# Optimization experiments

Hardware: AMD Instinct MI355X
Metric: run time of the kernel (lower is better)

Reference implementation:

```python
import jax, jax.numpy as jnp
import numpy as np

N_NODES = 1024
E_EDGES = 4096
P_DEG = 5


def setup_inputs() -> dict:
    rng = np.random.default_rng(0)
    N, E = N_NODES, E_EDGES
    # graph incidence matrix: column j has +1 at node n_j, -1 at node m_j
    n_idx = rng.integers(0, N, size=E)
    m_idx = (n_idx + 1 + rng.integers(0, N - 1, size=E)) % N  # guarantees n != m
    B = np.zeros((N, E), dtype=np.float32)
    B[n_idx, np.arange(E)] = 1.0
    B[m_idx, np.arange(E)] = -1.0
    edges = np.stack([n_idx, m_idx], axis=1).astype(np.int32)

    key = jax.random.key(0)
    kq, ky, ks = jax.random.split(key, 3)
    q = jax.random.normal(kq, (N,), dtype=jnp.float32)
    y = jax.random.normal(ky, (N,), dtype=jnp.float32)
    s0 = jax.random.uniform(ks, (E,), dtype=jnp.float32) + 0.1  # positive edge weights

    F = 0.99 * jnp.eye(E, dtype=jnp.float32)          # state transition (E x E)
    C_u = 1e-2 * jnp.eye(E, dtype=jnp.float32)        # process noise
    C_w = 1e-1 * jnp.eye(N, dtype=jnp.float32)        # measurement noise
    Sigma0 = jnp.eye(E, dtype=jnp.float32)            # initial state covariance
    a = jnp.array([0.0, 1.0, 0.5, 0.25, 0.1], dtype=jnp.float32)  # poly coeffs, P=5

    return {"q": q, "y": y, "F": F, "B": jnp.asarray(B), "edges": jnp.asarray(edges),
            "C_u": C_u, "C_w": C_w, "s0": s0, "Sigma0": Sigma0, "a": a}


def _ekf_step(q, y, F, B, edges, C_u, C_w, s0, Sigma0, a):
    N = q.shape[0]
    P = a.shape[0]
    dt = q.dtype

    # ---- predict ----
    s = F @ s0
    Sigma = F @ Sigma0 @ F.T + C_u

    # ---- update ----
    # L = B diag(s) B^T  (weighted graph Laplacian)
    L = (B * s[None, :]) @ B.T  # (N, N)

    # c[p] = L^p q  (forward recursion)
    def c_step(cp, _):
        cn = L @ cp
        return cn, cn
    _, cs = jax.lax.scan(c_step, q, None, length=P - 1)
    c = jnp.concatenate([q[None, :], cs], axis=0)  # (P, N)

    # D[P-1] = 0;  D[p] = L @ D[p+1] + a[p+1] * I  (backward recursion)
    I_N = jnp.eye(N, dtype=dt)
    def d_step(Dn, ap1):
        Dp = L @ Dn + ap1 * I_N
        return Dp, Dp
    _, Ds = jax.lax.scan(d_step, jnp.zeros((N, N), dtype=dt), a[1:][::-1])
    # Ds[k] = D[P-2-k] -> reorder to D[0..P-1], append D[P-1]=0
    D = jnp.concatenate([Ds[::-1], jnp.zeros((1, N, N), dtype=dt)], axis=0)  # (P, N, N)

    # edge-indexed gather, vectorized over all edges
    n_i = edges[:, 0]
    m_i = edges[:, 1]
    dc = c[:, n_i] - c[:, m_i]          # (P, E)
    dD = D[:, :, n_i] - D[:, :, m_i]    # (P, N, E)
    H = jnp.einsum('pe,pne->ne', dc, dD)  # Jacobian (N, E)

    # Kalman gain (solve instead of explicit inverse; S symmetric)
    S = H @ Sigma @ H.T + C_w                 # (N, N)
    PHt = Sigma @ H.T                          # (E, N)
    K = jnp.linalg.solve(S, PHt.T).T           # (E, N)

    # innovation uses compute_poly(L, q, a) = sum_p a_p L^p q = sum_p a_p c[p]
    f_pred = jnp.einsum('p,pn->n', a, c)
    s_new = s + K @ (y - f_pred)

    # Joseph-form covariance update (computed as in base class; not returned)
    I_E = jnp.eye(s.shape[0], dtype=dt)
    IKH = I_E - K @ H
    Sigma_new = IKH @ Sigma @ IKH.T + K @ C_w @ K.T

    s_out = jnp.maximum(s_new, 0.0)
    return s_out, Sigma_new


def reference(q, y, F, B, edges, C_u, C_w, s0, Sigma0, a):
    s_out, _ = _ekf_step(q, y, F, B, edges, C_u, C_w, s0, Sigma0, a)
    return s_out
```

## Files before the change

### kernel.cpp

```cpp
#include <hip/hip_runtime.h>

#define NN 1024
#define EE 4096
#define CAP 64
#define BD 64
#define NB 16
#define KSPLIT 4
#define NTILE 136
#define NSLOT 200
#define GFACT 122

__device__ __forceinline__ double waveReduceD(double v){
  for (int o = 32; o; o >>= 1) v += __shfl_down(v, o, 64);
  return v;
}
__device__ __forceinline__ double agld(const double* p){
  return __hip_atomic_load(p, __ATOMIC_RELAXED, __HIP_MEMORY_SCOPE_AGENT);
}
__device__ __forceinline__ void agst(double* p, double v){
  __hip_atomic_store(p, v, __ATOMIC_RELAXED, __HIP_MEMORY_SCOPE_AGENT);
}

__global__ __launch_bounds__(1024) void k_prep(const float* __restrict__ F, const float* __restrict__ Sg0,
                                               const float* __restrict__ Cu, const float* __restrict__ s0,
                                               const int* __restrict__ edges, const float* __restrict__ q,
                                               const float* __restrict__ y, const float* __restrict__ a,
                                               float* __restrict__ sv, float* __restrict__ sg,
                                               float* __restrict__ L, int* __restrict__ cnt,
                                               int* __restrict__ nb, float* __restrict__ wg,
                                               float* __restrict__ bt, double* __restrict__ rz){
  __shared__ int scnt[NN];
  __shared__ float cbs[5][NN];
  int tid = threadIdx.x;
  scnt[tid] = 0;
  __syncthreads();
  for (int e = tid; e < EE; e += 1024){
    float f = F[(size_t)e*EE + e];
    float se = f * s0[e];
    sv[e] = se;
    sg[e] = f*f*Sg0[(size_t)e*EE + e] + Cu[(size_t)e*EE + e];
    int n = edges[2*e], m = edges[2*e+1];
    atomicAdd(&L[(size_t)n*NN + n],  se);
    atomicAdd(&L[(size_t)m*NN + m],  se);
    atomicAdd(&L[(size_t)n*NN + m], -se);
    atomicAdd(&L[(size_t)m*NN + n], -se);
    int p1 = atomicAdd(&scnt[n], 1);
    if (p1 < CAP){ nb[n*CAP+p1] = m; wg[n*CAP+p1] = se; }
    int p2 = atomicAdd(&scnt[m], 1);
    if (p2 < CAP){ nb[m*CAP+p2] = n; wg[m*CAP+p2] = se; }
  }
  __syncthreads();
  cnt[tid] = scnt[tid];
  cbs[0][tid] = q[tid];
  __syncthreads();
  for (int p = 1; p < 5; ++p){
    float acc = L[(size_t)tid*NN + tid] * cbs[p-1][tid];
    int c = min(scnt[tid], CAP);
    for (int t = 0; t < c; ++t) acc -= wg[tid*CAP+t] * cbs[p-1][nb[tid*CAP+t]];
    cbs[p][tid] = acc;
    __syncthreads();
  }
  float a1 = a[1], a2 = a[2], a3 = a[3], a4 = a[4];
  for (int e = tid; e < EE; e += 1024){
    int n = edges[2*e], m = edges[2*e+1];
    float dc0 = cbs[0][n]-cbs[0][m], dc1 = cbs[1][n]-cbs[1][m];
    float dc2 = cbs[2][n]-cbs[2][m], dc3 = cbs[3][n]-cbs[3][m];
    bt[e]      = dc0*a1 + dc1*a2 + dc2*a3 + dc3*a4;
    bt[EE+e]   = dc0*a2 + dc1*a3 + dc2*a4;
    bt[2*EE+e] = dc0*a3 + dc1*a4;
    bt[3*EE+e] = dc0*a4;
  }
  double acc = (double)y[tid];
  float a0 = a[0];
  acc -= (double)a0*cbs[0][tid]; acc -= (double)a1*cbs[1][tid];
  acc -= (double)a2*cbs[2][tid]; acc -= (double)a3*cbs[3][tid];
  acc -= (double)a4*cbs[4][tid];
  rz[tid] = acc;
}

__global__ __launch_bounds__(256) void k_srow(const float* __restrict__ L, const int* __restrict__ cnt,
                                              const int* __restrict__ nb, const float* __restrict__ wg,
                                              const float* __restrict__ X, float* __restrict__ Y){
  int i = blockIdx.x;
  __shared__ int   snb[CAP];
  __shared__ float swt[CAP];
  __shared__ float sdiag;
  int c = min(cnt[i], CAP);
  if ((int)threadIdx.x < c){ snb[threadIdx.x] = nb[i*CAP+threadIdx.x]; swt[threadIdx.x] = wg[i*CAP+threadIdx.x]; }
  if (threadIdx.x == 0) sdiag = L[(size_t)i*NN + i];
  __syncthreads();
  for (int j = threadIdx.x; j < NN; j += 256){
    float acc = sdiag * X[(size_t)i*NN + j];
    for (int t = 0; t < c; ++t) acc -= swt[t] * X[(size_t)snb[t]*NN + j];
    Y[(size_t)i*NN + j] = acc;
  }
}

__global__ __launch_bounds__(256) void k_hbuild(const int* __restrict__ edges, const float* __restrict__ bt,
                                                const float* __restrict__ L, const float* __restrict__ L2,
                                                const float* __restrict__ L3, float* __restrict__ Ht){
  int e = blockIdx.x;
  int n = edges[2*e], m = edges[2*e+1];
  float b0 = bt[e], b1 = bt[EE+e], b2 = bt[2*EE+e], b3 = bt[3*EE+e];
  const float* Ln  = L  + (size_t)n*NN; const float* Lm  = L  + (size_t)m*NN;
  const float* L2n = L2 + (size_t)n*NN; const float* L2m = L2 + (size_t)m*NN;
  const float* L3n = L3 + (size_t)n*NN; const float* L3m = L3 + (size_t)m*NN;
  float* He = Ht + (size_t)e*NN;
  for (int j = threadIdx.x; j < NN; j += 256){
    float v = b1*(Ln[j]-Lm[j]) + b2*(L2n[j]-L2m[j]) + b3*(L3n[j]-L3m[j]);
    if (j == n) v += b0;
    if (j == m) v -= b0;
    He[j] = v;
  }
}

__device__ __forceinline__ void tri_decode(int p, int& ti, int& tj){
  ti = (int)((sqrtf(8.f*p + 1.f) - 1.f)*0.5f);
  while ((ti+1)*(ti+2)/2 <= p) ti++;
  while (ti*(ti+1)/2 > p) ti--;
  tj = p - ti*(ti+1)/2;
}

__global__ __launch_bounds__(256,2) void k_sgemm2(const float* __restrict__ Ht, const float* __restrict__ sg,
                                                  double* __restrict__ Spart){
  int p = blockIdx.x, z = blockIdx.y;
  int ti, tj; tri_decode(p, ti, tj);
  int i0 = ti*64, j0 = tj*64;
  __shared__ double As[32][66];
  __shared__ double Bs[32][66];
  int tid = threadIdx.x;
  int tx = tid & 15, ty = tid >> 4;
  double acc[4][4] = {};
  int kbase = z*(EE/KSPLIT);
  for (int k0 = kbase; k0 < kbase + EE/KSPLIT; k0 += 32){
#pragma unroll
    for (int l = 0; l < 2; ++l){
      int s = tid + 256*l;
      int kk = s >> 4, g = s & 15;
      const float* row = Ht + (size_t)(k0+kk)*NN;
      float4 va = *(const float4*)(row + i0 + g*4);
      float4 vb = *(const float4*)(row + j0 + g*4);
      double sgd = (double)sg[k0+kk];
      As[kk][g*4+0] = (double)va.x; As[kk][g*4+1] = (double)va.y;
      As[kk][g*4+2] = (double)va.z; As[kk][g*4+3] = (double)va.w;
      Bs[kk][g*4+0] = (double)vb.x*sgd; Bs[kk][g*4+1] = (double)vb.y*sgd;
      Bs[kk][g*4+2] = (double)vb.z*sgd; Bs[kk][g*4+3] = (double)vb.w*sgd;
    }
    __syncthreads();
#pragma unroll
    for (int kk = 0; kk < 32; ++kk){
      double av[4], bv[4];
#pragma unroll
      for (int q = 0; q < 4; ++q){ av[q] = As[kk][tx*4+q]; bv[q] = Bs[kk][ty*4+q]; }
#pragma unroll
      for (int r = 0; r < 4; ++r)
#pragma unroll
        for (int c = 0; c < 4; ++c)
          acc[r][c] += av[r]*bv[c];
    }
    __syncthreads();
  }
  double* out = Spart + ((size_t)z*NTILE + p)*4096;
#pragma unroll
  for (int r = 0; r < 4; ++r)
#pragma unroll
    for (int c = 0; c < 4; ++c)
      out[(tx*4+r)*64 + ty*4+c] = acc[r][c];
}

__global__ __launch_bounds__(256,1) void k_fact(const double* __restrict__ Spart, const float* __restrict__ Cw,
                                                double* __restrict__ Sd, double* __restrict__ rz,
                                                double* __restrict__ grd, double* __restrict__ dvals,
                                                int* __restrict__ fl){
  __shared__ double T[BD][BD+1];
  __shared__ double R[BD][BD+1];
  __shared__ double dsh[BD];
  __shared__ double zsh[BD];
  int bid = blockIdx.x, tid = threadIdx.x;
  int tx = tid & 15, ty = tid >> 4;
  int lane = tid & 63, wv = tid >> 6;

  auto poll_one = [&](int slot){
    int it = 0;
    while (__hip_atomic_load(&fl[slot*16], __ATOMIC_RELAXED, __HIP_MEMORY_SCOPE_AGENT) == 0 && it < 30000000){
      __builtin_amdgcn_s_sleep(2); ++it;
    }
  };
  auto wait2 = [&](int s1, int s2){
    if (tid == 0){ poll_one(s1); if (s2 >= 0) poll_one(s2); }
    __syncthreads();
  };
  auto set_slot = [&](int slot){
    __syncthreads();
    if (tid == 0)
      __hip_atomic_store(&fl[slot*16], 1, __ATOMIC_RELAXED, __HIP_MEMORY_SCOPE_AGENT);
  };
  auto pslotf = [](int X, int tt){ return (X == tt+1) ? (16+tt) : (32 + (X-1)*(X-2)/2 + tt); };

  auto load_acc = [&](int pidx, int gi, int gj, double (&acc)[4][4]){
    const double* sp = Spart + (size_t)pidx*4096;
#pragma unroll
    for (int q2 = 0; q2 < 4; ++q2)
#pragma unroll
      for (int p2 = 0; p2 < 4; ++p2){
        int idx = (tx*4+q2)*64 + ty*4+p2;
        double v = (double)Cw[(size_t)(gi+tx*4+q2)*NN + gj+ty*4+p2];
        v += sp[idx];
        v += sp[(size_t)NTILE*4096 + idx];
        v += sp[(size_t)2*NTILE*4096 + idx];
        v += sp[(size_t)3*NTILE*4096 + idx];
        acc[q2][p2] = v;
      }
  };
  auto upd = [&](double (&acc)[4][4]){
    for (int k = 0; k < BD; ++k){
      double av[4], bv[4];
#pragma unroll
      for (int q2 = 0; q2 < 4; ++q2){ av[q2] = T[tx*4+q2][k]; bv[q2] = R[ty*4+q2][k]; }
#pragma unroll
      for (int r = 0; r < 4; ++r)
#pragma unroll
        for (int c = 0; c < 4; ++c)
          acc[r][c] -= av[r]*bv[c];
    }
  };
  auto ldT = [&](int row64, int col64){
    for (int idx = tid; idx < 4096; idx += 256){
      int r = idx >> 6, c = idx & 63;
      T[r][c] = agld(&Sd[(size_t)(row64+r)*NN + col64 + c]);
    }
  };

  auto factor64 = [&](int off){
    if (tid < 64){
      double r_[64];
#pragma unroll
      for (int k = 0; k < 64; ++k) r_[k] = T[tid][k];
      double myd = 0.0;
#pragma unroll
      for (int j = 0; j < 64; ++j){
        double d = __shfl(r_[j], j, 64);
        double l = r_[j]/d;
        double lm = (tid > j) ? l : 0.0;
        if (tid == j) myd = d;
#pragma unroll
        for (int k = j+1; k < 64; ++k){
          double p = __shfl(r_[k], j, 64);
          r_[k] -= lm*p;
        }
        if (tid > j) r_[j] = l;
      }
      double myinv = 1.0/myd;
#pragma unroll
      for (int k = 0; k < 64; ++k) if (k > tid) r_[k] *= myinv;
#pragma unroll
      for (int k = 0; k < 64; ++k) T[tid][k] = r_[k];
      dsh[tid] = myinv;
      agst(&grd[off+tid], myinv);
      agst(&dvals[off+tid], myd);
    }
    __syncthreads();
  };
  auto trsm64 = [&](){
    if (tid < 64){
      double x_[64];
#pragma unroll
      for (int k = 0; k < 64; ++k) x_[k] = R[tid][k];
#pragma unroll
      for (int j = 1; j < 64; ++j){
        double a2 = x_[j];
#pragma unroll
        for (int k = 0; k < j; ++k) a2 -= x_[k]*T[j][k];
        x_[j] = a2;
      }
#pragma unroll
      for (int k = 0; k < 64; ++k) R[tid][k] = x_[k]*dsh[k];
    }
    __syncthreads();
  };

  if (bid < NB){
    int t = bid, t64 = t*64, u64 = t64+64;
    double accD[4][4], accP[4][4];
    load_acc(t*(t+1)/2 + t, t64, t64, accD);
    if (t < 15) load_acc((t+1)*(t+2)/2 + t, u64, t64, accP);
    for (int tt = 0; tt < t; ++tt){
      int tt64 = tt*64;
      wait2(pslotf(t,tt), -1);
      if (tid < 64) dsh[tid] = agld(&dvals[tt64+tid]);
      ldT(t64, tt64);
      __syncthreads();
      for (int idx = tid; idx < 4096; idx += 256){
        int r = idx >> 6, c = idx & 63;
        R[r][c] = T[r][c]*dsh[c];
      }
      __syncthreads();
      upd(accD);
      __syncthreads();
      if (t < 15){
        wait2(pslotf(t+1,tt), -1);
        ldT(u64, tt64);
        __syncthreads();
        upd(accP);
        __syncthreads();
      }
    }
#pragma unroll
    for (int q2 = 0; q2 < 4; ++q2)
#pragma unroll
      for (int p2 = 0; p2 < 4; ++p2) T[tx*4+q2][ty*4+p2] = accD[q2][p2];
    __syncthreads();
    factor64(t64);
    for (int idx = tid; idx < 4096; idx += 256){
      int r = idx >> 6, c = idx & 63;
      agst(&Sd[(size_t)(t64+r)*NN + t64 + c], T[r][c]);
    }
    set_slot(t);
    if (t < 15){
#pragma unroll
      for (int q2 = 0; q2 < 4; ++q2)
#pragma unroll
        for (int p2 = 0; p2 < 4; ++p2) R[tx*4+q2][ty*4+p2] = accP[q2][p2];
      __syncthreads();
      trsm64();
      for (int idx = tid; idx < 4096; idx += 256){
        int r = idx >> 6, c = idx & 63;
        agst(&Sd[(size_t)(u64+r)*NN + t64 + c], R[r][c]);
      }
      set_slot(16+t);
    }
  } else if (bid < NB + 105){
    int q = bid - NB;
    int I = 2;
    for (int ii = 3; ii <= 15; ++ii) if ((ii-1)*(ii-2)/2 <= q) I = ii;
    int J = q - (I-1)*(I-2)/2;
    int i64 = I*64, j64 = J*64;
    double acc[4][4];
    load_acc(I*(I+1)/2 + J, i64, j64, acc);
    for (int tt = 0; tt < J; ++tt){
      int tt64 = tt*64;
      wait2(pslotf(I,tt), pslotf(J,tt));
      if (tid < 64) dsh[tid] = agld(&dvals[tt64+tid]);
      __syncthreads();
      for (int idx = tid; idx < 4096; idx += 256){
        int r = idx >> 6, c = idx & 63;
        T[r][c] = agld(&Sd[(size_t)(i64+r)*NN + tt64 + c]);
        R[r][c] = agld(&Sd[(size_t)(j64+r)*NN + tt64 + c]) * dsh[c];
      }
      __syncthreads();
      upd(acc);
      __syncthreads();
    }
    wait2(J, -1);
    ldT(j64, j64);
    if (tid < 64) dsh[tid] = agld(&grd[j64+tid]);
    __syncthreads();
#pragma unroll
    for (int q2 = 0; q2 < 4; ++q2)
#pragma unroll
      for (int p2 = 0; p2 < 4; ++p2) R[tx*4+q2][ty*4+p2] = acc[q2][p2];
    __syncthreads();
    trsm64();
    for (int idx = tid; idx < 4096; idx += 256){
      int r = idx >> 6, c = idx & 63;
      agst(&Sd[(size_t)(i64+r)*NN + j64 + c], R[r][c]);
    }
    set_slot(32 + (I-1)*(I-2)/2 + J);
  } else {
    for (int t = 0; t < NB; ++t){
      int t64 = t*64;
      {
        int I = t+2+tid;
        if (I <= 15) poll_one(32 + (I-1)*(I-2)/2 + t);
        if (tid == 0){ poll_one(t); if (t < 15) poll_one(16+t); }
      }
      __syncthreads();
      for (int idx = tid; idx < BD*BD; idx += 256){
        int r = idx >> 6, c = idx & 63;
        T[r][c] = agld(&Sd[(size_t)(t64+r)*NN + t64 + c]);
      }
      __syncthreads();
      if (wv == 0){
        double x = rz[t64 + lane];
        for (int j = 0; j < BD-1; ++j){
          double xj = __shfl(x, j, 64);
          if (lane > j) x -= T[j][lane]*xj;
        }
        zsh[lane] = x;
        rz[t64 + lane] = x;
      }
      __syncthreads();
      for (int g0 = t64 + BD + wv*4; g0 < NN; g0 += 16){
        double v0 = agld(&Sd[(size_t)(g0+0)*NN + t64 + lane])*zsh[lane];
        double v1 = agld(&Sd[(size_t)(g0+1)*NN + t64 + lane])*zsh[lane];
        double v2 = agld(&Sd[(size_t)(g0+2)*NN + t64 + lane])*zsh[lane];
        double v3 = agld(&Sd[(size_t)(g0+3)*NN + t64 + lane])*zsh[lane];
        v0 = waveReduceD(v0); v1 = waveReduceD(v1);
        v2 = waveReduceD(v2); v3 = waveReduceD(v3);
        if (lane == 0){
          rz[g0+0] -= v0; rz[g0+1] -= v1; rz[g0+2] -= v2; rz[g0+3] -= v3;
        }
      }
      __syncthreads();
    }
    for (int i = tid; i < NN; i += 256) rz[i] *= agld(&grd[i]);
    __syncthreads();
    for (int t = NB-1; t >= 0; --t){
      int t64 = t*64;
      for (int idx = tid; idx < BD*BD; idx += 256){
        int r = idx >> 6, c = idx & 63;
        T[r][c] = agld(&Sd[(size_t)(t64+r)*NN + t64 + c]);
      }
      __syncthreads();
      if (wv == 0){
        double x = rz[t64 + lane];
        for (int j = BD-1; j >= 1; --j){
          double xj = __shfl(x, j, 64);
          if (lane < j) x -= T[j][lane]*xj;
        }
        zsh[lane] = x;
        rz[t64 + lane] = x;
      }
      __syncthreads();
      for (int J = wv; J < t; J += 4){
        int j64 = J*64;
        double a2 = 0.0;
#pragma unroll 8
        for (int r = 0; r < 64; ++r)
          a2 += agld(&Sd[(size_t)(t64+r)*NN + j64 + lane]) * zsh[r];
        rz[j64+lane] -= a2;
      }
      __syncthreads();
    }
  }
}

__global__ __launch_bounds__(256) void k_snew(const float* __restrict__ Ht, const float* __restrict__ sv,
                                              const float* __restrict__ sg, const double* __restrict__ z,
                                              float* __restrict__ out){
  int e = blockIdx.x*4 + (threadIdx.x >> 6);
  int lane = threadIdx.x & 63;
  const float* He = Ht + (size_t)e*NN;
  double acc = 0.0;
  for (int j = lane; j < NN; j += 64) acc += (double)He[j]*z[j];
  acc = waveReduceD(acc);
  if (lane == 0){
    double val = (double)sv[e] + (double)sg[e]*acc;
    out[e] = fmaxf((float)val, 0.0f);
  }
}

extern "C" void kernel_launch(void* const* d_in, const int* in_sizes, int n_in,
                              void* d_out, int out_size, void* d_ws, size_t ws_size,
                              hipStream_t stream){
  const float* q   = (const float*)d_in[0];
  const float* y   = (const float*)d_in[1];
  const float* F   = (const float*)d_in[2];
  const int*   edges = (const int*)d_in[4];
  const float* Cu  = (const float*)d_in[5];
  const float* Cw  = (const float*)d_in[6];
  const float* s0  = (const float*)d_in[7];
  const float* Sg0 = (const float*)d_in[8];
  const float* a   = (const float*)d_in[9];
  float* out = (float*)d_out;

  double* Sd    = (double*)d_ws;
  double* Spart = Sd + (size_t)NN*NN;
  double* rz    = Spart + (size_t)KSPLIT*NTILE*4096;
  double* grd   = rz + NN;
  double* dvals = grd + NN;
  float* w = (float*)(dvals + NN);
  float* L  = w; w += (size_t)NN*NN;
  float* L2 = w; w += (size_t)NN*NN;
  float* L3 = w; w += (size_t)NN*NN;
  float* Ht = w; w += (size_t)EE*NN;
  float* sv = w; w += EE;
  float* sg = w; w += EE;
  float* bt = w; w += 4*EE;
  float* wg = w; w += (size_t)NN*CAP;
  int* cnt  = (int*)w; w += NN;
  int* nb   = (int*)w; w += (size_t)NN*CAP;
  int* fl   = (int*)w; w += NSLOT*16;

  hipMemsetAsync(L, 0, (size_t)NN*NN*sizeof(float), stream);
  hipMemsetAsync(fl, 0, NSLOT*16*sizeof(int), stream);

  k_prep<<<1, 1024, 0, stream>>>(F, Sg0, Cu, s0, edges, q, y, a,
                                 sv, sg, L, cnt, nb, wg, bt, rz);

  k_srow<<<NN, 256, 0, stream>>>(L, cnt, nb, wg, L,  L2);
  k_srow<<<NN, 256, 0, stream>>>(L, cnt, nb, wg, L2, L3);
  k_hbuild<<<EE, 256, 0, stream>>>(edges, bt, L, L2, L3, Ht);

  dim3 gg(NTILE, KSPLIT);
  k_sgemm2<<<gg, 256, 0, stream>>>(Ht, sg, Spart);

  k_fact<<<GFACT, 256, 0, stream>>>(Spart, Cw, Sd, rz, grd, dvals, fl);

  k_snew<<<EE/4, 256, 0, stream>>>(Ht, sv, sg, rz, out);
}
```

Baseline: 1.639 ms.

## Widen factorization blocks to 1024 threads and split triangular solve into own kernel

The blocked LDL^T factorization kernel now runs 1024 threads per block, so each thread holds a 2x2 accumulator instead of 4x4 and the tile loads and stores are spread over more threads. The forward/backward triangular solve that used to run in a dedicated polling block overlapped with the factorization is moved to a separate single-block kernel launched afterward. That kernel uses 1024 threads and plain loads instead of atomic loads. This gives more parallelism per tile and removes the solve's flag polling. In exchange it loses the overlap of the solve with the factorization and adds one kernel launch. The factor64 and trsm64 helpers, which are only partly visible, still assume thread indices below 64 and must work with the larger blocks.

```diff
diff --git a/kernel.cpp b/kernel.cpp
--- a/kernel.cpp
+++ b/kernel.cpp
@@ -8,7 +8,7 @@
 #define KSPLIT 4
 #define NTILE 136
 #define NSLOT 200
-#define GFACT 122
+#define GFACT 121
 
 __device__ __forceinline__ double waveReduceD(double v){
   for (int o = 32; o; o >>= 1) v += __shfl_down(v, o, 64);
@@ -168,17 +168,15 @@
       out[(tx*4+r)*64 + ty*4+c] = acc[r][c];
 }
 
-__global__ __launch_bounds__(256,1) void k_fact(const double* __restrict__ Spart, const float* __restrict__ Cw,
-                                                double* __restrict__ Sd, double* __restrict__ rz,
-                                                double* __restrict__ grd, double* __restrict__ dvals,
-                                                int* __restrict__ fl){
+__global__ __launch_bounds__(1024,1) void k_fact(const double* __restrict__ Spart, const float* __restrict__ Cw,
+                                                 double* __restrict__ Sd,
+                                                 double* __restrict__ grd, double* __restrict__ dvals,
+                                                 int* __restrict__ fl){
   __shared__ double T[BD][BD+1];
   __shared__ double R[BD][BD+1];
   __shared__ double dsh[BD];
-  __shared__ double zsh[BD];
   int bid = blockIdx.x, tid = threadIdx.x;
-  int tx = tid & 15, ty = tid >> 4;
-  int lane = tid & 63, wv = tid >> 6;
+  int tx = tid & 31, ty = tid >> 5;
 
   auto poll_one = [&](int slot){
     int it = 0;
@@ -197,14 +195,14 @@
   };
   auto pslotf = [](int X, int tt){ return (X == tt+1) ? (16+tt) : (32 + (X-1)*(X-2)/2 + tt); };
 
-  auto load_acc = [&](int pidx, int gi, int gj, double (&acc)[4][4]){
+  auto load_acc = [&](int pidx, int gi, int gj, double (&acc)[2][2]){
     const double* sp = Spart + (size_t)pidx*4096;
 #pragma unroll
-    for (int q2 = 0; q2 < 4; ++q2)
-#pragma unroll
-      for (int p2 = 0; p2 < 4; ++p2){
-        int idx = (tx*4+q2)*64 + ty*4+p2;
-        double v = (double)Cw[(size_t)(gi+tx*4+q2)*NN + gj+ty*4+p2];
+    for (int q2 = 0; q2 < 2; ++q2)
+#pragma unroll
+      for (int p2 = 0; p2 < 2; ++p2){
+        int idx = (tx*2+q2)*64 + ty*2+p2;
+        double v = (double)Cw[(size_t)(gi+tx*2+q2)*NN + gj+ty*2+p2];
         v += sp[idx];
         v += sp[(size_t)NTILE*4096 + idx];
         v += sp[(size_t)2*NTILE*4096 + idx];
@@ -212,20 +210,20 @@
         acc[q2][p2] = v;
       }
   };
-  auto upd = [&](double (&acc)[4][4]){
+  auto upd = [&](double (&acc)[2][2]){
     for (int k = 0; k < BD; ++k){
-      double av[4], bv[4];
-#pragma unroll
-      for (int q2 = 0; q2 < 4; ++q2){ av[q2] = T[tx*4+q2][k]; bv[q2] = R[ty*4+q2][k]; }
-#pragma unroll
-      for (int r = 0; r < 4; ++r)
-#pragma unroll
-        for (int c = 0; c < 4; ++c)
+      double av[2], bv[2];
+#pragma unroll
+      for (int q2 = 0; q2 < 2; ++q2){ av[q2] = T[tx*2+q2][k]; bv[q2] = R[ty*2+q2][k]; }
+#pragma unroll
+      for (int r = 0; r < 2; ++r)
+#pragma unroll
+        for (int c = 0; c < 2; ++c)
           acc[r][c] -= av[r]*bv[c];
     }
   };
   auto ldT = [&](int row64, int col64){
-    for (int idx = tid; idx < 4096; idx += 256){
+    for (int idx = tid; idx < 4096; idx += 1024){
       int r = idx >> 6, c = idx & 63;
       T[r][c] = agld(&Sd[(size_t)(row64+r)*NN + col64 + c]);
     }
@@ -281,7 +279,7 @@
 
   if (bid < NB){
     int t = bid, t64 = t*64, u64 = t64+64;
-    double accD[4][4], accP[4][4];
+    double accD[2][2], accP[2][2];
     load_acc(t*(t+1)/2 + t, t64, t64, accD);
     if (t < 15) load_acc((t+1)*(t+2)/2 + t, u64, t64, accP);
     for (int tt = 0; tt < t; ++tt){
@@ -290,7 +288,7 @@
       if (tid < 64) dsh[tid] = agld(&dvals[tt64+tid]);
       ldT(t64, tt64);
       __syncthreads();
-      for (int idx = tid; idx < 4096; idx += 256){
+      for (int idx = tid; idx < 4096; idx += 1024){
         int r = idx >> 6, c = idx & 63;
         R[r][c] = T[r][c]*dsh[c];
       }
@@ -306,43 +304,43 @@
       }
     }
 #pragma unroll
-    for (int q2 = 0; q2 < 4; ++q2)
-#pragma unroll
-      for (int p2 = 0; p2 < 4; ++p2) T[tx*4+q2][ty*4+p2] = accD[q2][p2];
+    for (int q2 = 0; q2 < 2; ++q2)
+#pragma unroll
+      for (int p2 = 0; p2 < 2; ++p2) T[tx*2+q2][ty*2+p2] = accD[q2][p2];
     __syncthreads();
     factor64(t64);
-    for (int idx = tid; idx < 4096; idx += 256){
+    for (int idx = tid; idx < 4096; idx += 1024){
       int r = idx >> 6, c = idx & 63;
       agst(&Sd[(size_t)(t64+r)*NN + t64 + c], T[r][c]);
     }
     set_slot(t);
     if (t < 15){
 #pragma unroll
-      for (int q2 = 0; q2 < 4; ++q2)
-#pragma unroll
-        for (int p2 = 0; p2 < 4; ++p2) R[tx*4+q2][ty*4+p2] = accP[q2][p2];
+      for (int q2 = 0; q2 < 2; ++q2)
+#pragma unroll
+        for (int p2 = 0; p2 < 2; ++p2) R[tx*2+q2][ty*2+p2] = accP[q2][p2];
       __syncthreads();
       trsm64();
-      for (int idx = tid; idx < 4096; idx += 256){
+      for (int idx = tid; idx < 4096; idx += 1024){
         int r = idx >> 6, c = idx & 63;
         agst(&Sd[(size_t)(u64+r)*NN + t64 + c], R[r][c]);
       }
       set_slot(16+t);
     }
-  } else if (bid < NB + 105){
+  } else {
     int q = bid - NB;
     int I = 2;
     for (int ii = 3; ii <= 15; ++ii) if ((ii-1)*(ii-2)/2 <= q) I = ii;
     int J = q - (I-1)*(I-2)/2;
     int i64 = I*64, j64 = J*64;
-    double acc[4][4];
+    double acc[2][2];
     load_acc(I*(I+1)/2 + J, i64, j64, acc);
     for (int tt = 0; tt < J; ++tt){
       int tt64 = tt*64;
       wait2(pslotf(I,tt), pslotf(J,tt));
       if (tid < 64) dsh[tid] = agld(&dvals[tt64+tid]);
       __syncthreads();
-      for (int idx = tid; idx < 4096; idx += 256){
+      for (int idx = tid; idx < 4096; idx += 1024){
         int r = idx >> 6, c = idx & 63;
         T[r][c] = agld(&Sd[(size_t)(i64+r)*NN + tt64 + c]);
         R[r][c] = agld(&Sd[(size_t)(j64+r)*NN + tt64 + c]) * dsh[c];
@@ -356,82 +354,82 @@
     if (tid < 64) dsh[tid] = agld(&grd[j64+tid]);
     __syncthreads();
 #pragma unroll
-    for (int q2 = 0; q2 < 4; ++q2)
-#pragma unroll
-      for (int p2 = 0; p2 < 4; ++p2) R[tx*4+q2][ty*4+p2] = acc[q2][p2];
+    for (int q2 = 0; q2 < 2; ++q2)
+#pragma unroll
+      for (int p2 = 0; p2 < 2; ++p2) R[tx*2+q2][ty*2+p2] = acc[q2][p2];
     __syncthreads();
     trsm64();
-    for (int idx = tid; idx < 4096; idx += 256){
+    for (int idx = tid; idx < 4096; idx += 1024){
       int r = idx >> 6, c = idx & 63;
       agst(&Sd[(size_t)(i64+r)*NN + j64 + c], R[r][c]);
     }
     set_slot(32 + (I-1)*(I-2)/2 + J);
-  } else {
-    for (int t = 0; t < NB; ++t){
-      int t64 = t*64;
-      {
-        int I = t+2+tid;
-        if (I <= 15) poll_one(32 + (I-1)*(I-2)/2 + t);
-        if (tid == 0){ poll_one(t); if (t < 15) poll_one(16+t); }
-      }
-      __syncthreads();
-      for (int idx = tid; idx < BD*BD; idx += 256){
-        int r = idx >> 6, c = idx & 63;
-        T[r][c] = agld(&Sd[(size_t)(t64+r)*NN + t64 + c]);
-      }
-      __syncthreads();
-      if (wv == 0){
-        double x = rz[t64 + lane];
-        for (int j = 0; j < BD-1; ++j){
-          double xj = __shfl(x, j, 64);
-          if (lane > j) x -= T[j][lane]*xj;
-        }
-        zsh[lane] = x;
-        rz[t64 + lane] = x;
-      }
-      __syncthreads();
-      for (int g0 = t64 + BD + wv*4; g0 < NN; g0 += 16){
-        double v0 = agld(&Sd[(size_t)(g0+0)*NN + t64 + lane])*zsh[lane];
-        double v1 = agld(&Sd[(size_t)(g0+1)*NN + t64 + lane])*zsh[lane];
-        double v2 = agld(&Sd[(size_t)(g0+2)*NN + t64 + lane])*zsh[lane];
-        double v3 = agld(&Sd[(size_t)(g0+3)*NN + t64 + lane])*zsh[lane];
-        v0 = waveReduceD(v0); v1 = waveReduceD(v1);
-        v2 = waveReduceD(v2); v3 = waveReduceD(v3);
-        if (lane == 0){
-          rz[g0+0] -= v0; rz[g0+1] -= v1; rz[g0+2] -= v2; rz[g0+3] -= v3;
-        }
-      }
-      __syncthreads();
-    }
-    for (int i = tid; i < NN; i += 256) rz[i] *= agld(&grd[i]);
-    __syncthreads();
-    for (int t = NB-1; t >= 0; --t){
-      int t64 = t*64;
-      for (int idx = tid; idx < BD*BD; idx += 256){
-        int r = idx >> 6, c = idx & 63;
-        T[r][c] = agld(&Sd[(size_t)(t64+r)*NN + t64 + c]);
-      }
-      __syncthreads();
-      if (wv == 0){
-        double x = rz[t64 + lane];
-        for (int j = BD-1; j >= 1; --j){
-          double xj = __shfl(x, j, 64);
-          if (lane < j) x -= T[j][lane]*xj;
-        }
-        zsh[lane] = x;
-        rz[t64 + lane] = x;
-      }
-      __syncthreads();
-      for (int J = wv; J < t; J += 4){
-        int j64 = J*64;
-        double a2 = 0.0;
+  }
+}
+
+__global__ __launch_bounds__(1024) void k_solve(const double* __restrict__ Sd, double* __restrict__ rz,
+                                                const double* __restrict__ grd){
+  __shared__ double T[BD][BD+1];
+  __shared__ double zsh[BD];
+  int tid = threadIdx.x, lane = tid & 63, wv = tid >> 6;
+  for (int t = 0; t < NB; ++t){
+    int t64 = t*64;
+    for (int idx = tid; idx < BD*BD; idx += 1024){
+      int r = idx >> 6, c = idx & 63;
+      T[r][c] = Sd[(size_t)(t64+r)*NN + t64 + c];
+    }
+    __syncthreads();
+    if (wv == 0){
+      double x = rz[t64 + lane];
+      for (int j = 0; j < BD-1; ++j){
+        double xj = __shfl(x, j, 64);
+        if (lane > j) x -= T[j][lane]*xj;
+      }
+      zsh[lane] = x;
+      rz[t64 + lane] = x;
+    }
+    __syncthreads();
+    for (int g0 = t64 + BD + wv*4; g0 < NN; g0 += 64){
+      double v0 = Sd[(size_t)(g0+0)*NN + t64 + lane]*zsh[lane];
+      double v1 = Sd[(size_t)(g0+1)*NN + t64 + lane]*zsh[lane];
+      double v2 = Sd[(size_t)(g0+2)*NN + t64 + lane]*zsh[lane];
+      double v3 = Sd[(size_t)(g0+3)*NN + t64 + lane]*zsh[lane];
+      v0 = waveReduceD(v0); v1 = waveReduceD(v1);
+      v2 = waveReduceD(v2); v3 = waveReduceD(v3);
+      if (lane == 0){
+        rz[g0+0] -= v0; rz[g0+1] -= v1; rz[g0+2] -= v2; rz[g0+3] -= v3;
+      }
+    }
+    __syncthreads();
+  }
+  rz[tid] *= grd[tid];
+  __syncthreads();
+  for (int t = NB-1; t >= 0; --t){
+    int t64 = t*64;
+    for (int idx = tid; idx < BD*BD; idx += 1024){
+      int r = idx >> 6, c = idx & 63;
+      T[r][c] = Sd[(size_t)(t64+r)*NN + t64 + c];
+    }
+    __syncthreads();
+    if (wv == 0){
+      double x = rz[t64 + lane];
+      for (int j = BD-1; j >= 1; --j){
+        double xj = __shfl(x, j, 64);
+        if (lane < j) x -= T[j][lane]*xj;
+      }
+      zsh[lane] = x;
+      rz[t64 + lane] = x;
+    }
+    __syncthreads();
+    for (int J = wv; J < t; J += 16){
+      int j64 = J*64;
+      double a2 = 0.0;
 #pragma unroll 8
-        for (int r = 0; r < 64; ++r)
-          a2 += agld(&Sd[(size_t)(t64+r)*NN + j64 + lane]) * zsh[r];
-        rz[j64+lane] -= a2;
-      }
-      __syncthreads();
-    }
+      for (int r = 0; r < 64; ++r)
+        a2 += Sd[(size_t)(t64+r)*NN + j64 + lane] * zsh[r];
+      rz[j64+lane] -= a2;
+    }
+    __syncthreads();
   }
 }
 
@@ -495,7 +493,8 @@
   dim3 gg(NTILE, KSPLIT);
   k_sgemm2<<<gg, 256, 0, stream>>>(Ht, sg, Spart);
 
-  k_fact<<<GFACT, 256, 0, stream>>>(Spart, Cw, Sd, rz, grd, dvals, fl);
+  k_fact<<<GFACT, 1024, 0, stream>>>(Spart, Cw, Sd, grd, dvals, fl);
+  k_solve<<<1, 1024, 0, stream>>>(Sd, rz, grd);
 
   k_snew<<<EE/4, 256, 0, stream>>>(Ht, sv, sg, rz, out);
 }
```

Measured after the change: 4.481 ms. 2.73x slower.

## Parallelize block LDL factor and trsm across block, split triangular solve into own kernel

Applied to the files above, without the earlier changes.

Replaces the single-wave register-resident 64x64 LDL factorization and triangular solve with versions that use all 256 threads through shared memory, in the column-chunked trsm form. Diagonal blocks now publish their factor before accumulating the sub-diagonal panel, which shortens the dependency chain for the other blocks. The forward and backward solve moves out of the persistent fused kernel into a separate 1024-thread launch, removing polling and atomic loads from that path. The cost is an extra kernel launch and more barriers inside the factor loop.

```diff
diff --git a/kernel.cpp b/kernel.cpp
--- a/kernel.cpp
+++ b/kernel.cpp
@@ -8,7 +8,7 @@
 #define KSPLIT 4
 #define NTILE 136
 #define NSLOT 200
-#define GFACT 122
+#define GFACT 121
 
 __device__ __forceinline__ double waveReduceD(double v){
   for (int o = 32; o; o >>= 1) v += __shfl_down(v, o, 64);
@@ -169,16 +169,14 @@
 }
 
 __global__ __launch_bounds__(256,1) void k_fact(const double* __restrict__ Spart, const float* __restrict__ Cw,
-                                                double* __restrict__ Sd, double* __restrict__ rz,
+                                                double* __restrict__ Sd,
                                                 double* __restrict__ grd, double* __restrict__ dvals,
                                                 int* __restrict__ fl){
   __shared__ double T[BD][BD+1];
   __shared__ double R[BD][BD+1];
   __shared__ double dsh[BD];
-  __shared__ double zsh[BD];
   int bid = blockIdx.x, tid = threadIdx.x;
   int tx = tid & 15, ty = tid >> 4;
-  int lane = tid & 63, wv = tid >> 6;
 
   auto poll_one = [&](int slot){
     int it = 0;
@@ -231,52 +229,48 @@
     }
   };
 
-  auto factor64 = [&](int off){
-    if (tid < 64){
-      double r_[64];
-#pragma unroll
-      for (int k = 0; k < 64; ++k) r_[k] = T[tid][k];
-      double myd = 0.0;
-#pragma unroll
-      for (int j = 0; j < 64; ++j){
-        double d = __shfl(r_[j], j, 64);
-        double l = r_[j]/d;
-        double lm = (tid > j) ? l : 0.0;
-        if (tid == j) myd = d;
-#pragma unroll
-        for (int k = j+1; k < 64; ++k){
-          double p = __shfl(r_[k], j, 64);
-          r_[k] -= lm*p;
+  auto factor_wb = [&](int off0){
+    __syncthreads();
+    for (int j = 0; j < BD; ++j){
+      double dj = T[j][j];
+      int fi = tid & 63, cg = tid >> 6;
+      if (fi > j){
+        double l = T[j][fi]/dj;
+        for (int c = j+1+cg; c < BD; c += 4) T[fi][c] -= l*T[j][c];
+      }
+      __syncthreads();
+    }
+    if (tid < BD) dsh[tid] = 1.0 / T[tid][tid];
+    __syncthreads();
+    for (int idx = tid; idx < BD*BD; idx += 256){
+      int r = idx >> 6, c = idx & 63;
+      double v = (r == c) ? T[r][r] : (r > c ? T[r][c]*dsh[c] : T[r][c]*dsh[r]);
+      agst(&Sd[(size_t)(off0+r)*NN + off0 + c], v);
+    }
+    if (tid < BD){ agst(&grd[off0+tid], dsh[tid]); agst(&dvals[off0+tid], 1.0/dsh[tid]); }
+  };
+  auto trsm_chunk = [&](){
+    for (int c0 = 0; c0 < BD; c0 += 16){
+      if (tid < BD){
+        for (int jj = 0; jj < 16; ++jj){
+          int j = c0 + jj;
+          double a2 = R[tid][j];
+          for (int k = 0; k < jj; ++k) a2 -= R[tid][c0+k]*T[j][c0+k];
+          R[tid][j] = a2;
         }
-        if (tid > j) r_[j] = l;
-      }
-      double myinv = 1.0/myd;
-#pragma unroll
-      for (int k = 0; k < 64; ++k) if (k > tid) r_[k] *= myinv;
-#pragma unroll
-      for (int k = 0; k < 64; ++k) T[tid][k] = r_[k];
-      dsh[tid] = myinv;
-      agst(&grd[off+tid], myinv);
-      agst(&dvals[off+tid], myd);
-    }
-    __syncthreads();
-  };
-  auto trsm64 = [&](){
-    if (tid < 64){
-      double x_[64];
-#pragma unroll
-      for (int k = 0; k < 64; ++k) x_[k] = R[tid][k];
-#pragma unroll
-      for (int j = 1; j < 64; ++j){
-        double a2 = x_[j];
-#pragma unroll
-        for (int k = 0; k < j; ++k) a2 -= x_[k]*T[j][k];
-        x_[j] = a2;
-      }
-#pragma unroll
-      for (int k = 0; k < 64; ++k) R[tid][k] = x_[k]*dsh[k];
-    }
-    __syncthreads();
+      }
+      __syncthreads();
+      if (c0 + 16 < BD){
+        int r2 = tid & 63, jg = tid >> 6;
+        for (int j = c0+16+jg; j < BD; j += 4){
+          double a2 = R[r2][j];
+#pragma unroll
+          for (int k = 0; k < 16; ++k) a2 -= R[r2][c0+k]*T[j][c0+k];
+          R[r2][j] = a2;
+        }
+        __syncthreads();
+      }
+    }
   };
 
   if (bid < NB){
@@ -297,39 +291,44 @@
       __syncthreads();
       upd(accD);
       __syncthreads();
-      if (t < 15){
+    }
+#pragma unroll
+    for (int q2 = 0; q2 < 4; ++q2)
+#pragma unroll
+      for (int p2 = 0; p2 < 4; ++p2) T[tx*4+q2][ty*4+p2] = accD[q2][p2];
+    factor_wb(t64);
+    set_slot(t);
+    if (t < 15){
+      for (int tt = 0; tt < t; ++tt){
+        int tt64 = tt*64;
         wait2(pslotf(t+1,tt), -1);
-        ldT(u64, tt64);
+        if (tid < 64) dsh[tid] = agld(&dvals[tt64+tid]);
+        __syncthreads();
+        for (int idx = tid; idx < 4096; idx += 256){
+          int r = idx >> 6, c = idx & 63;
+          T[r][c] = agld(&Sd[(size_t)(u64+r)*NN + tt64 + c]);
+          R[r][c] = agld(&Sd[(size_t)(t64+r)*NN + tt64 + c]) * dsh[c];
+        }
         __syncthreads();
         upd(accP);
         __syncthreads();
       }
-    }
-#pragma unroll
-    for (int q2 = 0; q2 < 4; ++q2)
-#pragma unroll
-      for (int p2 = 0; p2 < 4; ++p2) T[tx*4+q2][ty*4+p2] = accD[q2][p2];
-    __syncthreads();
-    factor64(t64);
-    for (int idx = tid; idx < 4096; idx += 256){
-      int r = idx >> 6, c = idx & 63;
-      agst(&Sd[(size_t)(t64+r)*NN + t64 + c], T[r][c]);
-    }
-    set_slot(t);
-    if (t < 15){
+      ldT(t64, t64);
+      if (tid < 64) dsh[tid] = agld(&grd[t64+tid]);
+      __syncthreads();
 #pragma unroll
       for (int q2 = 0; q2 < 4; ++q2)
 #pragma unroll
         for (int p2 = 0; p2 < 4; ++p2) R[tx*4+q2][ty*4+p2] = accP[q2][p2];
       __syncthreads();
-      trsm64();
+      trsm_chunk();
       for (int idx = tid; idx < 4096; idx += 256){
         int r = idx >> 6, c = idx & 63;
-        agst(&Sd[(size_t)(u64+r)*NN + t64 + c], R[r][c]);
+        agst(&Sd[(size_t)(u64+r)*NN + t64 + c], R[r][c]*dsh[c]);
       }
       set_slot(16+t);
     }
-  } else if (bid < NB + 105){
+  } else {
     int q = bid - NB;
     int I = 2;
     for (int ii = 3; ii <= 15; ++ii) if ((ii-1)*(ii-2)/2 <= q) I = ii;
@@ -360,78 +359,78 @@
 #pragma unroll
       for (int p2 = 0; p2 < 4; ++p2) R[tx*4+q2][ty*4+p2] = acc[q2][p2];
     __syncthreads();
-    trsm64();
+    trsm_chunk();
     for (int idx = tid; idx < 4096; idx += 256){
       int r = idx >> 6, c = idx & 63;
-      agst(&Sd[(size_t)(i64+r)*NN + j64 + c], R[r][c]);
+      agst(&Sd[(size_t)(i64+r)*NN + j64 + c], R[r][c]*dsh[c]);
     }
     set_slot(32 + (I-1)*(I-2)/2 + J);
-  } else {
-    for (int t = 0; t < NB; ++t){
-      int t64 = t*64;
-      {
-        int I = t+2+tid;
-        if (I <= 15) poll_one(32 + (I-1)*(I-2)/2 + t);
-        if (tid == 0){ poll_one(t); if (t < 15) poll_one(16+t); }
-      }
-      __syncthreads();
-      for (int idx = tid; idx < BD*BD; idx += 256){
-        int r = idx >> 6, c = idx & 63;
-        T[r][c] = agld(&Sd[(size_t)(t64+r)*NN + t64 + c]);
-      }
-      __syncthreads();
-      if (wv == 0){
-        double x = rz[t64 + lane];
-        for (int j = 0; j < BD-1; ++j){
-          double xj = __shfl(x, j, 64);
-          if (lane > j) x -= T[j][lane]*xj;
-        }
-        zsh[lane] = x;
-        rz[t64 + lane] = x;
-      }
-      __syncthreads();
-      for (int g0 = t64 + BD + wv*4; g0 < NN; g0 += 16){
-        double v0 = agld(&Sd[(size_t)(g0+0)*NN + t64 + lane])*zsh[lane];
-        double v1 = agld(&Sd[(size_t)(g0+1)*NN + t64 + lane])*zsh[lane];
-        double v2 = agld(&Sd[(size_t)(g0+2)*NN + t64 + lane])*zsh[lane];
-        double v3 = agld(&Sd[(size_t)(g0+3)*NN + t64 + lane])*zsh[lane];
-        v0 = waveReduceD(v0); v1 = waveReduceD(v1);
-        v2 = waveReduceD(v2); v3 = waveReduceD(v3);
-        if (lane == 0){
-          rz[g0+0] -= v0; rz[g0+1] -= v1; rz[g0+2] -= v2; rz[g0+3] -= v3;
-        }
-      }
-      __syncthreads();
-    }
-    for (int i = tid; i < NN; i += 256) rz[i] *= agld(&grd[i]);
-    __syncthreads();
-    for (int t = NB-1; t >= 0; --t){
-      int t64 = t*64;
-      for (int idx = tid; idx < BD*BD; idx += 256){
-        int r = idx >> 6, c = idx & 63;
-        T[r][c] = agld(&Sd[(size_t)(t64+r)*NN + t64 + c]);
-      }
-      __syncthreads();
-      if (wv == 0){
-        double x = rz[t64 + lane];
-        for (int j = BD-1; j >= 1; --j){
-          double xj = __shfl(x, j, 64);
-          if (lane < j) x -= T[j][lane]*xj;
-        }
-        zsh[lane] = x;
-        rz[t64 + lane] = x;
-      }
-      __syncthreads();
-      for (int J = wv; J < t; J += 4){
-        int j64 = J*64;
-        double a2 = 0.0;
+  }
+}
+
+__global__ __launch_bounds__(1024) void k_solve(const double* __restrict__ Sd, double* __restrict__ rz,
+                                                const double* __restrict__ grd){
+  __shared__ double T[BD][BD+1];
+  __shared__ double zsh[BD];
+  int tid = threadIdx.x, lane = tid & 63, wv = tid >> 6;
+  for (int t = 0; t < NB; ++t){
+    int t64 = t*64;
+    for (int idx = tid; idx < BD*BD; idx += 1024){
+      int r = idx >> 6, c = idx & 63;
+      T[r][c] = Sd[(size_t)(t64+r)*NN + t64 + c];
+    }
+    __syncthreads();
+    if (wv == 0){
+      double x = rz[t64 + lane];
+      for (int j = 0; j < BD-1; ++j){
+        double xj = __shfl(x, j, 64);
+        if (lane > j) x -= T[j][lane]*xj;
+      }
+      zsh[lane] = x;
+      rz[t64 + lane] = x;
+    }
+    __syncthreads();
+    for (int g0 = t64 + BD + wv*4; g0 < NN; g0 += 64){
+      double v0 = Sd[(size_t)(g0+0)*NN + t64 + lane]*zsh[lane];
+      double v1 = Sd[(size_t)(g0+1)*NN + t64 + lane]*zsh[lane];
+      double v2 = Sd[(size_t)(g0+2)*NN + t64 + lane]*zsh[lane];
+      double v3 = Sd[(size_t)(g0+3)*NN + t64 + lane]*zsh[lane];
+      v0 = waveReduceD(v0); v1 = waveReduceD(v1);
+      v2 = waveReduceD(v2); v3 = waveReduceD(v3);
+      if (lane == 0){
+        rz[g0+0] -= v0; rz[g0+1] -= v1; rz[g0+2] -= v2; rz[g0+3] -= v3;
+      }
+    }
+    __syncthreads();
+  }
+  rz[tid] *= grd[tid];
+  __syncthreads();
+  for (int t = NB-1; t >= 0; --t){
+    int t64 = t*64;
+    for (int idx = tid; idx < BD*BD; idx += 1024){
+      int r = idx >> 6, c = idx & 63;
+      T[r][c] = Sd[(size_t)(t64+r)*NN + t64 + c];
+    }
+    __syncthreads();
+    if (wv == 0){
+      double x = rz[t64 + lane];
+      for (int j = BD-1; j >= 1; --j){
+        double xj = __shfl(x, j, 64);
+        if (lane < j) x -= T[j][lane]*xj;
+      }
+      zsh[lane] = x;
+      rz[t64 + lane] = x;
+    }
+    __syncthreads();
+    for (int J = wv; J < t; J += 16){
+      int j64 = J*64;
+      double a2 = 0.0;
 #pragma unroll 8
-        for (int r = 0; r < 64; ++r)
-          a2 += agld(&Sd[(size_t)(t64+r)*NN + j64 + lane]) * zsh[r];
-        rz[j64+lane] -= a2;
-      }
-      __syncthreads();
-    }
+      for (int r = 0; r < 64; ++r)
+        a2 += Sd[(size_t)(t64+r)*NN + j64 + lane] * zsh[r];
+      rz[j64+lane] -= a2;
+    }
+    __syncthreads();
   }
 }
 
@@ -495,7 +494,8 @@
   dim3 gg(NTILE, KSPLIT);
   k_sgemm2<<<gg, 256, 0, stream>>>(Ht, sg, Spart);
 
-  k_fact<<<GFACT, 256, 0, stream>>>(Spart, Cw, Sd, rz, grd, dvals, fl);
+  k_fact<<<GFACT, 256, 0, stream>>>(Spart, Cw, Sd, grd, dvals, fl);
+  k_solve<<<1, 1024, 0, stream>>>(Sd, rz, grd);
 
   k_snew<<<EE/4, 256, 0, stream>>>(Ht, sv, sg, rz, out);
 }
```

After: 3.002 ms. 83.2% more time.
